# Kernel tuning notes

Measured on AMD Instinct MI355X. Metric: run time of the kernel, lower is better.

The kernel has to match this reference:

```python
import jax, jax.numpy as jnp
import numpy as np

N_ANCHORS = 25
N_CLASSES = 16
X_IMG = 296
Y_IMG = 296
OPLIST = ['conv','conv','MP','conv','conv','MP','conv','conv','conv','MP','conv','conv','conv','MP','conv','conv','conv']

def _size_list(s):
    out = [s]
    for op in OPLIST:
        out.append(out[-1] - 2 if op == 'conv' else out[-1] // 2)
    return out

XLIST = _size_list(X_IMG)  # ends at 7
YLIST = _size_list(Y_IMG)
FEAT = XLIST[-1]           # final feature-map size (7)
GRID = XLIST[-1] - 2       # anchor grid (5), source's xlist[-1]-2 convention
B, C = 2, 512


def setup_inputs() -> dict:
    key = jax.random.key(0)
    ks = jax.random.split(key, 12)
    D = C * 49
    return {
        'cfeats':   jax.random.normal(ks[0], (B, C, FEAT, FEAT), jnp.float32),
        'regcls':   jax.random.normal(ks[1], (B, 5, N_ANCHORS, GRID, GRID), jnp.float32) * 0.5,
        'wanchors': jax.random.uniform(ks[2], (N_ANCHORS, GRID, GRID), jnp.float32, 16.0, 128.0),
        'hanchors': jax.random.uniform(ks[3], (N_ANCHORS, GRID, GRID), jnp.float32, 16.0, 128.0),
        'xanchors': jax.random.uniform(ks[4], (N_ANCHORS, GRID, GRID), jnp.float32, 0.0, float(X_IMG)),
        'yanchors': jax.random.uniform(ks[5], (N_ANCHORS, GRID, GRID), jnp.float32, 0.0, float(Y_IMG)),
        'w1': jax.random.normal(ks[6], (200, D), jnp.float32) * 0.02,
        'b1': jnp.zeros((200,), jnp.float32),
        'w2': jax.random.normal(ks[7], (100, 200), jnp.float32) * 0.02,
        'b2': jnp.zeros((100,), jnp.float32),
        'w3': jax.random.normal(ks[8], (N_CLASSES + 1, 100), jnp.float32) * 0.02,
        'b3': jnp.zeros((N_CLASSES + 1,), jnp.float32),
        'w4': jax.random.normal(ks[9], (4 * (N_CLASSES + 1), 100), jnp.float32) * 0.02,
        'b4': jnp.zeros((4 * (N_CLASSES + 1),), jnp.float32),
    }


def _forward(cfeats, regcls, wanchors, hanchors, xanchors, yanchors,
             w1, b1, w2, b2, w3, b3, w4, b4):
    Bq, Cq, Fq, _ = cfeats.shape
    A, G = N_ANCHORS, GRID
    # ---- anchor-box decode ----
    wreg = jnp.exp(regcls[:, 2]) * wanchors
    hreg = jnp.exp(regcls[:, 3]) * hanchors
    xreg = regcls[:, 0] * wanchors + xanchors
    yreg = regcls[:, 1] * hanchors + yanchors
    xis = xreg - wreg / 2.0
    yis = yreg - hreg / 2.0
    xfs = xreg + wreg / 2.0
    yfs = yreg + hreg / 2.0
    c0 = jnp.floor(jax.nn.relu(xis))
    c1 = jnp.floor(jax.nn.relu(yis))
    c2 = jnp.minimum(jnp.ceil(xfs), float(X_IMG - 1))
    c3 = jnp.maximum(jnp.ceil(yfs), float(Y_IMG - 1))  # (sic) max, as in source
    valid = (xis < float(X_IMG)) & (yis < float(Y_IMG)) & (xfs >= 0.0) & (yfs >= 0.0)
    c4 = jnp.where(valid, jax.nn.sigmoid(regcls[:, 4]), 0.0)
    # ---- track coords through the conv/MP stack ----
    for i, op in enumerate(OPLIST):
        if op == 'conv':
            c0 = jax.nn.relu(c0 - 1.0)
            c1 = jax.nn.relu(c1 - 1.0)
            c2 = jnp.minimum(c2, float(XLIST[i + 1] - 1))
            c3 = jnp.minimum(c3, float(YLIST[i + 1] - 1))
        else:
            c0 = jnp.floor(c0 / 2.0); c1 = jnp.floor(c1 / 2.0)
            c2 = jnp.floor(c2 / 2.0); c3 = jnp.floor(c3 / 2.0)
    N = A * G * G  # flatten (anchor, x, y) -> roi index, same order as source
    xi = c0.reshape(Bq, N).astype(jnp.int32)
    yi = c1.reshape(Bq, N).astype(jnp.int32)
    xf = c2.reshape(Bq, N).astype(jnp.int32)
    yf = c3.reshape(Bq, N).astype(jnp.int32)
    roi_on = c4.reshape(Bq, N) > 0.0
    # ---- 7x7 RoIPool (vectorized; bins partition [xi, xf+1) via floor boundaries) ----
    ii = jnp.arange(8, dtype=jnp.int32)
    wx = xf + 1 - xi
    wy = yf + 1 - yi
    bx = xi[:, :, None] + (ii * wx[:, :, None]) // 7  # [B,N,8]
    by = yi[:, :, None] + (ii * wy[:, :, None]) // 7
    xs = jnp.arange(Fq, dtype=jnp.int32)
    maskx = (xs[None, None, None, :] >= bx[:, :, :7, None]) & (xs[None, None, None, :] < bx[:, :, 1:, None])  # [B,N,7,F]
    masky = (xs[None, None, None, :] >= by[:, :, :7, None]) & (xs[None, None, None, :] < by[:, :, 1:, None])
    NEG = jnp.float32(-1e30)
    feats_sg = jax.lax.stop_gradient(cfeats)
    # stage 1: max over x per bin i  -> val1/arg1: [B,N,7,C,F]
    val1 = jnp.full((Bq, N, 7, Cq, Fq), NEG, jnp.float32)
    arg1 = jnp.zeros((Bq, N, 7, Cq, Fq), jnp.int32)
    for x in range(Fq):
        cand = jnp.where(maskx[:, :, :, x][..., None, None], feats_sg[:, None, None, :, x, :], NEG)
        upd = cand > val1
        val1 = jnp.where(upd, cand, val1)
        arg1 = jnp.where(upd, x, arg1)
    # stage 2: max over y per bin j  -> val2/arg2: [B,N,7,7,C]
    val2 = jnp.full((Bq, N, 7, 7, Cq), NEG, jnp.float32)
    arg2 = jnp.zeros((Bq, N, 7, 7, Cq), jnp.int32)
    for y in range(Fq):
        cand = jnp.where(masky[:, :, None, :, y][..., None], val1[:, :, :, None, :, y], NEG)
        upd = cand > val2
        val2 = jnp.where(upd, cand, val2)
        arg2 = jnp.where(upd, y, arg2)
    # recover x index of the per-bin argmax, then one differentiable gather
    argx = jnp.take_along_axis(arg1[:, :, :, None, :, :], arg2[..., None], axis=-1)[..., 0]  # [B,N,7,7,C]
    cell = argx * Fq + arg2
    feats_flat = cfeats.reshape(Bq, Cq, Fq * Fq)
    pooled = jnp.take_along_axis(feats_flat[:, None, None, None, :, :], cell[..., None], axis=-1)[..., 0]
    keep = (val2 > NEG * 0.5) & roi_on[:, :, None, None, None]
    pooled = jnp.where(keep, pooled, 0.0)  # [B,N,7,7,C]
    # layout [..., C*49] with 49 = 7*i + j, matching source
    pooled = jnp.transpose(pooled, (0, 1, 4, 2, 3)).reshape(Bq, A, G, G, Cq * 49)
    # ---- MLP head ----
    z = jax.nn.relu(pooled @ w1.T + b1)
    z = jax.nn.relu(z @ w2.T + b2)
    z1 = z @ w3.T + b3
    z2 = z @ w4.T + b4
    K = N_CLASSES + 1
    z3 = jnp.stack([z2[..., 0:K], z2[..., K:2 * K], z2[..., 2 * K:3 * K], z2[..., 3 * K:4 * K]], axis=1)
    return z1, z3


def reference(cfeats, regcls, wanchors, hanchors, xanchors, yanchors,
              w1, b1, w2, b2, w3, b3, w4, b4):
    return _forward(cfeats, regcls, wanchors, hanchors, xanchors, yanchors,
                    w1, b1, w2, b2, w3, b3, w4, b4)
```

## Files before the change

kernel.cpp:

```cpp
#include <hip/hip_runtime.h>
#include <cstdint>

using short8 = __attribute__((ext_vector_type(8))) short;
using f32x4  = __attribute__((ext_vector_type(4))) float;

__device__ __forceinline__ uint16_t f2bf(float x) {
    uint32_t u = __float_as_uint(x);
    uint32_t r = (u + 0x7FFFu + ((u >> 16) & 1u)) >> 16;
    return (uint16_t)r;
}
__device__ __forceinline__ int fdiv7(int a) {
    int q = a / 7;
    if ((a % 7 != 0) && (a < 0)) q--;
    return q;
}

__global__ void __launch_bounds__(256) k_prep(const float* __restrict__ regcls,
                                              const float* __restrict__ wan,
                                              const float* __restrict__ han,
                                              const float* __restrict__ xan,
                                              const float* __restrict__ yan,
                                              const float* __restrict__ cf,
                                              const float* __restrict__ w1,
                                              const float* __restrict__ w2,
                                              const float* __restrict__ w3,
                                              const float* __restrict__ w4,
                                              int8_t* __restrict__ cells,
                                              uint16_t* __restrict__ cfb,
                                              uint16_t* __restrict__ w1f,
                                              float* __restrict__ w2t,
                                              float* __restrict__ w34t) {
    __shared__ float lds[16 * 804];
    int blk = blockIdx.x;
    int t = threadIdx.x;

    if (blk < 5) {
        int r = blk * 256 + t;
        if (r >= 1250) return;
        int b = r / 625, n = r - b * 625;
        const float* rc = regcls + b * 3125 + n;
        float t0 = rc[0], t1 = rc[625], t2 = rc[1250], t3 = rc[1875];
        float wa = wan[n], ha = han[n], xa = xan[n], ya = yan[n];
        float wr = expf(t2) * wa, hr = expf(t3) * ha;
        float xr = t0 * wa + xa, yr = t1 * ha + ya;
        float xis = xr - wr * 0.5f, yis = yr - hr * 0.5f;
        float xfs = xr + wr * 0.5f, yfs = yr + hr * 0.5f;
        bool valid = (xis < 296.f) && (yis < 296.f) && (xfs >= 0.f) && (yfs >= 0.f);
        int c0 = (int)floorf(fmaxf(xis, 0.f));
        int c1 = (int)floorf(fmaxf(yis, 0.f));
        int c2 = (int)fminf(ceilf(xfs), 295.f);
        int c3 = (int)fmaxf(ceilf(yfs), 295.f);
        const int  XL1[17]    = {294,292,146,144,142,71,69,67,65,32,30,28,26,13,11,9,7};
        const bool ISCONV[17] = {1,1,0,1,1,0,1,1,1,0,1,1,1,0,1,1,1};
        #pragma unroll
        for (int i = 0; i < 17; i++) {
            if (ISCONV[i]) {
                c0 = max(c0 - 1, 0); c1 = max(c1 - 1, 0);
                c2 = min(c2, XL1[i] - 1); c3 = min(c3, XL1[i] - 1);
            } else {
                c0 >>= 1; c1 >>= 1; c2 >>= 1; c3 >>= 1;
            }
        }
        int xi = c0, yi = c1, xf = c2, yf = c3;
        int wx = xf + 1 - xi, wy = yf + 1 - yi;
        int bx[8], by[8];
        #pragma unroll
        for (int i = 0; i < 8; i++) { bx[i] = xi + fdiv7(i * wx); by[i] = yi + fdiv7(i * wy); }
        int8_t* cr = cells + r * 64;
        #pragma unroll
        for (int i = 0; i < 7; i++)
            #pragma unroll
            for (int j = 0; j < 7; j++) {
                bool ne = valid && (bx[i + 1] > bx[i]) && (by[j + 1] > by[j]);
                cr[i * 7 + j] = ne ? (int8_t)(bx[i] * 7 + by[j]) : (int8_t)(-1);
            }
    } else if (blk < 37) {
        int g = (blk - 5) * 256 + t;
        int b = g >> 12;
        int xy = (g >> 6) & 63;
        int c0 = (g & 63) * 8;
        uint32_t pk[4];
        if (xy < 49) {
            #pragma unroll
            for (int h = 0; h < 4; h++) {
                uint16_t lo = f2bf(cf[(b * 512 + c0 + 2 * h) * 49 + xy]);
                uint16_t hi = f2bf(cf[(b * 512 + c0 + 2 * h + 1) * 49 + xy]);
                pk[h] = (uint32_t)lo | ((uint32_t)hi << 16);
            }
        } else {
            pk[0] = pk[1] = pk[2] = pk[3] = 0;
        }
        ((uint4*)cfb)[(b * 64 + xy) * 64 + (g & 63)] = make_uint4(pk[0], pk[1], pk[2], pk[3]);
    } else if (blk < 175) {
        int g = (blk - 37) * 256 + t;
        if (g < 200 * 128) {
            int k = g >> 7, o = g & 127;
            w2t[g] = (o < 100) ? w2[o * 200 + k] : 0.f;
        }
        int u = g - 200 * 128;
        if (u >= 0 && u < 100 * 96) {
            int k = u / 96, o = u - k * 96;
            float v = 0.f;
            if (o < 17) v = w3[o * 100 + k];
            else if (o < 85) v = w4[(o - 17) * 100 + k];
            w34t[u] = v;
        }
    } else {
        int idx = blk - 175;
        int nt = idx % 13, ct = idx / 13;
        int kbase = ct * 784;
        #pragma unroll 4
        for (int r = 0; r < 16; r++) {
            int o = nt * 16 + r;
            if (t < 196) {
                float4 v = make_float4(0.f, 0.f, 0.f, 0.f);
                if (o < 200) v = ((const float4*)(w1 + (size_t)o * 25088 + kbase))[t];
                *(float4*)&lds[r * 804 + 4 * t] = v;
            }
        }
        __syncthreads();
        int kc = ct >> 1;
        int q0 = (ct & 1) * 2;
        int lsub = t & 31;
        int l = q0 * 16 + lsub;
        int rrow = lsub & 15;
        int clbase = (lsub >> 4) * 8;
        for (int binb = 0; binb < 49; binb += 8) {
            int bin = binb + (t >> 5);
            if (bin < 49) {
                uint32_t pk[4];
                #pragma unroll
                for (int h = 0; h < 4; h++) {
                    uint16_t lo = f2bf(lds[rrow * 804 + (clbase + 2 * h) * 49 + bin]);
                    uint16_t hi = f2bf(lds[rrow * 804 + (clbase + 2 * h + 1) * 49 + bin]);
                    pk[h] = (uint32_t)lo | ((uint32_t)hi << 16);
                }
                ((uint4*)w1f)[((bin * 16 + kc) * 13 + nt) * 64 + l] =
                    make_uint4(pk[0], pk[1], pk[2], pk[3]);
            }
        }
    }
}

__global__ void __launch_bounds__(256) k_qgemm(const uint16_t* __restrict__ cfb,
                                               const uint16_t* __restrict__ w1f,
                                               float* __restrict__ Q) {
    __shared__ uint4 bs[16 * 64];
    int bin = blockIdx.x, nt = blockIdx.y;
    int t = threadIdx.x;
    const uint4* bw = (const uint4*)w1f + (bin * 208 + nt) * 64;
    for (int i = t; i < 16 * 64; i += 256) {
        int kc = i >> 6, l = i & 63;
        bs[i] = bw[kc * 832 + l];
    }
    __syncthreads();
    int w = t >> 6, l = t & 63;
    int r16 = l & 15, quad = l >> 4;
    int o = nt * 16 + r16;
    int xybase = w * 16 + quad * 4;
    #pragma unroll
    for (int b = 0; b < 2; b++) {
        const uint4* ap = (const uint4*)cfb + (b * 64 + w * 16 + r16) * 64 + quad;
        f32x4 acc = {0.f, 0.f, 0.f, 0.f};
        #pragma unroll
        for (int kc = 0; kc < 16; kc++) {
            uint4 av = ap[kc * 4];
            uint4 bv = bs[kc * 64 + l];
            short8 a8 = __builtin_bit_cast(short8, av);
            short8 b8 = __builtin_bit_cast(short8, bv);
            acc = __builtin_amdgcn_mfma_f32_16x16x32_bf16(a8, b8, acc, 0, 0, 0);
        }
        float* qb = Q + ((size_t)(b * 49 + bin) * 49) * 208 + o;
        #pragma unroll
        for (int reg = 0; reg < 4; reg++) {
            int xy = xybase + reg;
            if (xy < 49) qb[xy * 208] = acc[reg];
        }
    }
}

__global__ void __launch_bounds__(256) k_head(const int8_t* __restrict__ cells,
                                              const float* __restrict__ Q,
                                              const float* __restrict__ b1,
                                              const float* __restrict__ w2t,
                                              const float* __restrict__ b2,
                                              const float* __restrict__ w34t,
                                              const float* __restrict__ b3,
                                              const float* __restrict__ b4,
                                              float* __restrict__ out) {
    __shared__ float z1[200];
    __shared__ float z2[100];
    int r = blockIdx.x;
    int b = r / 625, n = r - b * 625;
    int t = threadIdx.x;
    const int8_t* cr = cells + r * 64;
    float s = 0.f;
    if (t < 208) {
        const float* qb = Q + (size_t)(b * 49) * 49 * 208 + t;
        #pragma unroll
        for (int bin = 0; bin < 49; bin++) {
            int cv = (int)cr[bin];
            int idx = max(cv, 0);
            float m = (cv >= 0) ? 1.f : 0.f;
            s += m * qb[(bin * 49 + idx) * 208];
        }
    }
    if (t < 200) z1[t] = fmaxf(s + b1[t], 0.f);
    __syncthreads();
    if (t < 100) {
        float a = b2[t];
        #pragma unroll 4
        for (int k = 0; k < 200; k++) a += z1[k] * w2t[k * 128 + t];
        z2[t] = fmaxf(a, 0.f);
    }
    __syncthreads();
    if (t < 85) {
        float a = (t < 17) ? b3[t] : b4[t - 17];
        #pragma unroll 4
        for (int k = 0; k < 100; k++) a += z2[k] * w34t[k * 96 + t];
        if (t < 17) {
            out[b * 10625 + n * 17 + t] = a;
        } else {
            int q = (t - 17) / 17, kk = (t - 17) - q * 17;
            out[21250 + b * 42500 + q * 10625 + n * 17 + kk] = a;
        }
    }
}

extern "C" void kernel_launch(void* const* d_in, const int* in_sizes, int n_in,
                              void* d_out, int out_size, void* d_ws, size_t ws_size,
                              hipStream_t stream) {
    const float* cfeats = (const float*)d_in[0];
    const float* regcls = (const float*)d_in[1];
    const float* wan    = (const float*)d_in[2];
    const float* han    = (const float*)d_in[3];
    const float* xan    = (const float*)d_in[4];
    const float* yan    = (const float*)d_in[5];
    const float* w1     = (const float*)d_in[6];
    const float* b1     = (const float*)d_in[7];
    const float* w2     = (const float*)d_in[8];
    const float* b2     = (const float*)d_in[9];
    const float* w3     = (const float*)d_in[10];
    const float* b3     = (const float*)d_in[11];
    const float* w4     = (const float*)d_in[12];
    const float* b4     = (const float*)d_in[13];

    char* ws = (char*)d_ws;
    int8_t*   cells = (int8_t*)ws;
    uint16_t* cfb   = (uint16_t*)(ws + 80000);
    uint16_t* w1f   = (uint16_t*)(ws + 211072);
    float*    Q     = (float*)(ws + 10647680);
    float*    w2t   = (float*)(ws + 14642944);
    float*    w34t  = (float*)(ws + 14745344);
    float*    out   = (float*)d_out;

    k_prep<<<dim3(591), dim3(256), 0, stream>>>(regcls, wan, han, xan, yan,
                                                cfeats, w1, w2, w3, w4,
                                                cells, cfb, w1f, w2t, w34t);
    k_qgemm<<<dim3(49, 13), dim3(256), 0, stream>>>(cfb, w1f, Q);
    k_head<<<dim3(1250), dim3(256), 0, stream>>>(cells, Q, b1, w2t, b2, w34t, b3, b4, out);
}
```

Measured before the change: 145.2 us.

## Fuse three kernels into one persistent kernel with grid-wide atomic barriers

```diff
diff --git a/kernel.cpp b/kernel.cpp
--- a/kernel.cpp
+++ b/kernel.cpp
@@ -15,214 +15,247 @@
     return q;
 }
 
-__global__ void __launch_bounds__(256) k_prep(const float* __restrict__ regcls,
-                                              const float* __restrict__ wan,
-                                              const float* __restrict__ han,
-                                              const float* __restrict__ xan,
-                                              const float* __restrict__ yan,
-                                              const float* __restrict__ cf,
-                                              const float* __restrict__ w1,
-                                              const float* __restrict__ w2,
-                                              const float* __restrict__ w3,
-                                              const float* __restrict__ w4,
-                                              int8_t* __restrict__ cells,
-                                              uint16_t* __restrict__ cfb,
-                                              uint16_t* __restrict__ w1f,
-                                              float* __restrict__ w2t,
-                                              float* __restrict__ w34t) {
-    __shared__ float lds[16 * 804];
-    int blk = blockIdx.x;
-    int t = threadIdx.x;
-
-    if (blk < 5) {
-        int r = blk * 256 + t;
-        if (r >= 1250) return;
-        int b = r / 625, n = r - b * 625;
-        const float* rc = regcls + b * 3125 + n;
-        float t0 = rc[0], t1 = rc[625], t2 = rc[1250], t3 = rc[1875];
-        float wa = wan[n], ha = han[n], xa = xan[n], ya = yan[n];
-        float wr = expf(t2) * wa, hr = expf(t3) * ha;
-        float xr = t0 * wa + xa, yr = t1 * ha + ya;
-        float xis = xr - wr * 0.5f, yis = yr - hr * 0.5f;
-        float xfs = xr + wr * 0.5f, yfs = yr + hr * 0.5f;
-        bool valid = (xis < 296.f) && (yis < 296.f) && (xfs >= 0.f) && (yfs >= 0.f);
-        int c0 = (int)floorf(fmaxf(xis, 0.f));
-        int c1 = (int)floorf(fmaxf(yis, 0.f));
-        int c2 = (int)fminf(ceilf(xfs), 295.f);
-        int c3 = (int)fmaxf(ceilf(yfs), 295.f);
-        const int  XL1[17]    = {294,292,146,144,142,71,69,67,65,32,30,28,26,13,11,9,7};
-        const bool ISCONV[17] = {1,1,0,1,1,0,1,1,1,0,1,1,1,0,1,1,1};
-        #pragma unroll
-        for (int i = 0; i < 17; i++) {
-            if (ISCONV[i]) {
-                c0 = max(c0 - 1, 0); c1 = max(c1 - 1, 0);
-                c2 = min(c2, XL1[i] - 1); c3 = min(c3, XL1[i] - 1);
+__device__ __forceinline__ void gbar(int* ctr, int target) {
+    __syncthreads();
+    if (threadIdx.x == 0) {
+        __threadfence_system();
+        __hip_atomic_fetch_add(ctr, 1, __ATOMIC_RELAXED, __HIP_MEMORY_SCOPE_SYSTEM);
+        int guard = 0;
+        while (__hip_atomic_load(ctr, __ATOMIC_RELAXED, __HIP_MEMORY_SCOPE_SYSTEM) < target) {
+            __builtin_amdgcn_s_sleep(1);
+            if (++guard > (1 << 27)) break;
+        }
+        __threadfence_system();
+    }
+    __syncthreads();
+}
+
+__global__ void __launch_bounds__(256, 2)
+k_fused(const float* __restrict__ regcls, const float* __restrict__ wan,
+        const float* __restrict__ han, const float* __restrict__ xan,
+        const float* __restrict__ yan, const float* __restrict__ cf,
+        const float* __restrict__ w1, const float* __restrict__ b1,
+        const float* __restrict__ w2, const float* __restrict__ b2,
+        const float* __restrict__ w3, const float* __restrict__ b3,
+        const float* __restrict__ w4, const float* __restrict__ b4,
+        int8_t* __restrict__ cells, uint16_t* __restrict__ cfb,
+        uint16_t* __restrict__ w1f, float* __restrict__ Q,
+        float* __restrict__ w2t, float* __restrict__ w34t,
+        int* __restrict__ bar, float* __restrict__ out)
+{
+    __shared__ __align__(16) char smem[16 * 788 * 2];
+    const int t = threadIdx.x;
+    const int nblk = gridDim.x;
+
+    for (int u = blockIdx.x; u < 591; u += nblk) {
+        if (u < 5) {
+            int r = u * 256 + t;
+            if (r < 1250) {
+                int b = r / 625, n = r - b * 625;
+                const float* rc = regcls + b * 3125 + n;
+                float t0 = rc[0], t1 = rc[625], t2 = rc[1250], t3 = rc[1875];
+                float wa = wan[n], ha = han[n], xa = xan[n], ya = yan[n];
+                float wr = expf(t2) * wa, hr = expf(t3) * ha;
+                float xr = t0 * wa + xa, yr = t1 * ha + ya;
+                float xis = xr - wr * 0.5f, yis = yr - hr * 0.5f;
+                float xfs = xr + wr * 0.5f, yfs = yr + hr * 0.5f;
+                bool valid = (xis < 296.f) && (yis < 296.f) && (xfs >= 0.f) && (yfs >= 0.f);
+                int c0 = (int)floorf(fmaxf(xis, 0.f));
+                int c1 = (int)floorf(fmaxf(yis, 0.f));
+                int c2 = (int)fminf(ceilf(xfs), 295.f);
+                int c3 = (int)fmaxf(ceilf(yfs), 295.f);
+                const int  XL1[17]    = {294,292,146,144,142,71,69,67,65,32,30,28,26,13,11,9,7};
+                const bool ISCONV[17] = {1,1,0,1,1,0,1,1,1,0,1,1,1,0,1,1,1};
+                #pragma unroll
+                for (int i = 0; i < 17; i++) {
+                    if (ISCONV[i]) {
+                        c0 = max(c0 - 1, 0); c1 = max(c1 - 1, 0);
+                        c2 = min(c2, XL1[i] - 1); c3 = min(c3, XL1[i] - 1);
+                    } else {
+                        c0 >>= 1; c1 >>= 1; c2 >>= 1; c3 >>= 1;
+                    }
+                }
+                int xi = c0, yi = c1, xf = c2, yf = c3;
+                int wx = xf + 1 - xi, wy = yf + 1 - yi;
+                int bx[8], by[8];
+                #pragma unroll
+                for (int i = 0; i < 8; i++) { bx[i] = xi + fdiv7(i * wx); by[i] = yi + fdiv7(i * wy); }
+                int8_t* crw = cells + r * 64;
+                #pragma unroll
+                for (int i = 0; i < 7; i++)
+                    #pragma unroll
+                    for (int j = 0; j < 7; j++) {
+                        bool ne = valid && (bx[i + 1] > bx[i]) && (by[j + 1] > by[j]);
+                        crw[i * 7 + j] = ne ? (int8_t)(bx[i] * 7 + by[j]) : (int8_t)(-1);
+                    }
+            }
+        } else if (u < 37) {
+            int g = (u - 5) * 256 + t;
+            int b = g >> 12;
+            int xy = (g >> 6) & 63;
+            int c0 = (g & 63) * 8;
+            uint32_t pk[4];
+            if (xy < 49) {
+                #pragma unroll
+                for (int h = 0; h < 4; h++) {
+                    uint16_t lo = f2bf(cf[(b * 512 + c0 + 2 * h) * 49 + xy]);
+                    uint16_t hi = f2bf(cf[(b * 512 + c0 + 2 * h + 1) * 49 + xy]);
+                    pk[h] = (uint32_t)lo | ((uint32_t)hi << 16);
+                }
             } else {
-                c0 >>= 1; c1 >>= 1; c2 >>= 1; c3 >>= 1;
-            }
-        }
-        int xi = c0, yi = c1, xf = c2, yf = c3;
-        int wx = xf + 1 - xi, wy = yf + 1 - yi;
-        int bx[8], by[8];
-        #pragma unroll
-        for (int i = 0; i < 8; i++) { bx[i] = xi + fdiv7(i * wx); by[i] = yi + fdiv7(i * wy); }
-        int8_t* cr = cells + r * 64;
-        #pragma unroll
-        for (int i = 0; i < 7; i++)
+                pk[0] = pk[1] = pk[2] = pk[3] = 0;
+            }
+            ((uint4*)cfb)[(b * 64 + xy) * 64 + (g & 63)] = make_uint4(pk[0], pk[1], pk[2], pk[3]);
+        } else if (u < 175) {
+            int g = (u - 37) * 256 + t;
+            if (g < 200 * 128) {
+                int k = g >> 7, o = g & 127;
+                w2t[g] = (o < 100) ? w2[o * 200 + k] : 0.f;
+            }
+            int uu = g - 200 * 128;
+            if (uu >= 0 && uu < 100 * 96) {
+                int k = uu / 96, o = uu - k * 96;
+                float v = 0.f;
+                if (o < 17) v = w3[o * 100 + k];
+                else if (o < 85) v = w4[(o - 17) * 100 + k];
+                w34t[uu] = v;
+            }
+        } else {
+            uint16_t* lh = (uint16_t*)smem;
+            __syncthreads();
+            int idx = u - 175;
+            int nt = idx % 13, ct = idx / 13;
+            int kbase = ct * 784;
+            #pragma unroll 4
+            for (int rr = 0; rr < 16; rr++) {
+                int o = nt * 16 + rr;
+                if (t < 196) {
+                    float4 v = make_float4(0.f, 0.f, 0.f, 0.f);
+                    if (o < 200) v = ((const float4*)(w1 + (size_t)o * 25088 + kbase))[t];
+                    ushort4 hv;
+                    hv.x = f2bf(v.x); hv.y = f2bf(v.y); hv.z = f2bf(v.z); hv.w = f2bf(v.w);
+                    *(ushort4*)&lh[rr * 788 + 4 * t] = hv;
+                }
+            }
+            __syncthreads();
+            int kc = ct >> 1;
+            int q0 = (ct & 1) * 2;
+            int lsub = t & 31;
+            int l = q0 * 16 + lsub;
+            int rrow = lsub & 15;
+            int clbase = (lsub >> 4) * 8;
+            for (int binb = 0; binb < 49; binb += 8) {
+                int bin = binb + (t >> 5);
+                if (bin < 49) {
+                    uint32_t pk[4];
+                    #pragma unroll
+                    for (int h = 0; h < 4; h++) {
+                        uint32_t lo = lh[rrow * 788 + (clbase + 2 * h) * 49 + bin];
+                        uint32_t hi = lh[rrow * 788 + (clbase + 2 * h + 1) * 49 + bin];
+                        pk[h] = lo | (hi << 16);
+                    }
+                    ((uint4*)w1f)[((bin * 16 + kc) * 13 + nt) * 64 + l] =
+                        make_uint4(pk[0], pk[1], pk[2], pk[3]);
+                }
+            }
+        }
+    }
+    gbar(bar, nblk);
+
+    {
+        uint4* bs = (uint4*)smem;
+        for (int u = blockIdx.x; u < 637; u += nblk) {
+            int bin = u % 49, nt = u / 49;
+            __syncthreads();
+            const uint4* bw = (const uint4*)w1f + (bin * 208 + nt) * 64;
+            for (int i = t; i < 16 * 64; i += 256) {
+                int kc = i >> 6, l = i & 63;
+                bs[i] = bw[kc * 832 + l];
+            }
+            __syncthreads();
+            int w = t >> 6, l = t & 63;
+            int r16 = l & 15, quad = l >> 4;
+            int o = nt * 16 + r16;
+            int xybase = w * 16 + quad * 4;
             #pragma unroll
-            for (int j = 0; j < 7; j++) {
-                bool ne = valid && (bx[i + 1] > bx[i]) && (by[j + 1] > by[j]);
-                cr[i * 7 + j] = ne ? (int8_t)(bx[i] * 7 + by[j]) : (int8_t)(-1);
-            }
-    } else if (blk < 37) {
-        int g = (blk - 5) * 256 + t;
-        int b = g >> 12;
-        int xy = (g >> 6) & 63;
-        int c0 = (g & 63) * 8;
-        uint32_t pk[4];
-        if (xy < 49) {
-            #pragma unroll
-            for (int h = 0; h < 4; h++) {
-                uint16_t lo = f2bf(cf[(b * 512 + c0 + 2 * h) * 49 + xy]);
-                uint16_t hi = f2bf(cf[(b * 512 + c0 + 2 * h + 1) * 49 + xy]);
-                pk[h] = (uint32_t)lo | ((uint32_t)hi << 16);
-            }
-        } else {
-            pk[0] = pk[1] = pk[2] = pk[3] = 0;
-        }
-        ((uint4*)cfb)[(b * 64 + xy) * 64 + (g & 63)] = make_uint4(pk[0], pk[1], pk[2], pk[3]);
-    } else if (blk < 175) {
-        int g = (blk - 37) * 256 + t;
-        if (g < 200 * 128) {
-            int k = g >> 7, o = g & 127;
-            w2t[g] = (o < 100) ? w2[o * 200 + k] : 0.f;
-        }
-        int u = g - 200 * 128;
-        if (u >= 0 && u < 100 * 96) {
-            int k = u / 96, o = u - k * 96;
-            float v = 0.f;
-            if (o < 17) v = w3[o * 100 + k];
-            else if (o < 85) v = w4[(o - 17) * 100 + k];
-            w34t[u] = v;
-        }
-    } else {
-        int idx = blk - 175;
-        int nt = idx % 13, ct = idx / 13;
-        int kbase = ct * 784;
-        #pragma unroll 4
-        for (int r = 0; r < 16; r++) {
-            int o = nt * 16 + r;
-            if (t < 196) {
-                float4 v = make_float4(0.f, 0.f, 0.f, 0.f);
-                if (o < 200) v = ((const float4*)(w1 + (size_t)o * 25088 + kbase))[t];
-                *(float4*)&lds[r * 804 + 4 * t] = v;
-            }
-        }
-        __syncthreads();
-        int kc = ct >> 1;
-        int q0 = (ct & 1) * 2;
-        int lsub = t & 31;
-        int l = q0 * 16 + lsub;
-        int rrow = lsub & 15;
-        int clbase = (lsub >> 4) * 8;
-        for (int binb = 0; binb < 49; binb += 8) {
-            int bin = binb + (t >> 5);
-            if (bin < 49) {
-                uint32_t pk[4];
-                #pragma unroll
-                for (int h = 0; h < 4; h++) {
-                    uint16_t lo = f2bf(lds[rrow * 804 + (clbase + 2 * h) * 49 + bin]);
-                    uint16_t hi = f2bf(lds[rrow * 804 + (clbase + 2 * h + 1) * 49 + bin]);
-                    pk[h] = (uint32_t)lo | ((uint32_t)hi << 16);
-                }
-                ((uint4*)w1f)[((bin * 16 + kc) * 13 + nt) * 64 + l] =
-                    make_uint4(pk[0], pk[1], pk[2], pk[3]);
-            }
-        }
-    }
-}
-
-__global__ void __launch_bounds__(256) k_qgemm(const uint16_t* __restrict__ cfb,
-                                               const uint16_t* __restrict__ w1f,
-                                               float* __restrict__ Q) {
-    __shared__ uint4 bs[16 * 64];
-    int bin = blockIdx.x, nt = blockIdx.y;
-    int t = threadIdx.x;
-    const uint4* bw = (const uint4*)w1f + (bin * 208 + nt) * 64;
-    for (int i = t; i < 16 * 64; i += 256) {
-        int kc = i >> 6, l = i & 63;
-        bs[i] = bw[kc * 832 + l];
-    }
-    __syncthreads();
-    int w = t >> 6, l = t & 63;
-    int r16 = l & 15, quad = l >> 4;
-    int o = nt * 16 + r16;
-    int xybase = w * 16 + quad * 4;
-    #pragma unroll
-    for (int b = 0; b < 2; b++) {
-        const uint4* ap = (const uint4*)cfb + (b * 64 + w * 16 + r16) * 64 + quad;
-        f32x4 acc = {0.f, 0.f, 0.f, 0.f};
-        #pragma unroll
-        for (int kc = 0; kc < 16; kc++) {
-            uint4 av = ap[kc * 4];
-            uint4 bv = bs[kc * 64 + l];
-            short8 a8 = __builtin_bit_cast(short8, av);
-            short8 b8 = __builtin_bit_cast(short8, bv);
-            acc = __builtin_amdgcn_mfma_f32_16x16x32_bf16(a8, b8, acc, 0, 0, 0);
-        }
-        float* qb = Q + ((size_t)(b * 49 + bin) * 49) * 208 + o;
-        #pragma unroll
-        for (int reg = 0; reg < 4; reg++) {
-            int xy = xybase + reg;
-            if (xy < 49) qb[xy * 208] = acc[reg];
-        }
-    }
-}
-
-__global__ void __launch_bounds__(256) k_head(const int8_t* __restrict__ cells,
-                                              const float* __restrict__ Q,
-                                              const float* __restrict__ b1,
-                                              const float* __restrict__ w2t,
-                                              const float* __restrict__ b2,
-                                              const float* __restrict__ w34t,
-                                              const float* __restrict__ b3,
-                                              const float* __restrict__ b4,
-                                              float* __restrict__ out) {
-    __shared__ float z1[200];
-    __shared__ float z2[100];
-    int r = blockIdx.x;
-    int b = r / 625, n = r - b * 625;
-    int t = threadIdx.x;
-    const int8_t* cr = cells + r * 64;
-    float s = 0.f;
-    if (t < 208) {
-        const float* qb = Q + (size_t)(b * 49) * 49 * 208 + t;
-        #pragma unroll
-        for (int bin = 0; bin < 49; bin++) {
-            int cv = (int)cr[bin];
-            int idx = max(cv, 0);
-            float m = (cv >= 0) ? 1.f : 0.f;
-            s += m * qb[(bin * 49 + idx) * 208];
-        }
-    }
-    if (t < 200) z1[t] = fmaxf(s + b1[t], 0.f);
-    __syncthreads();
-    if (t < 100) {
-        float a = b2[t];
-        #pragma unroll 4
-        for (int k = 0; k < 200; k++) a += z1[k] * w2t[k * 128 + t];
-        z2[t] = fmaxf(a, 0.f);
-    }
-    __syncthreads();
-    if (t < 85) {
-        float a = (t < 17) ? b3[t] : b4[t - 17];
-        #pragma unroll 4
-        for (int k = 0; k < 100; k++) a += z2[k] * w34t[k * 96 + t];
-        if (t < 17) {
-            out[b * 10625 + n * 17 + t] = a;
-        } else {
-            int q = (t - 17) / 17, kk = (t - 17) - q * 17;
-            out[21250 + b * 42500 + q * 10625 + n * 17 + kk] = a;
+            for (int b = 0; b < 2; b++) {
+                const uint4* ap = (const uint4*)cfb + (b * 64 + w * 16 + r16) * 64 + quad;
+                f32x4 acc = {0.f, 0.f, 0.f, 0.f};
+                #pragma unroll
+                for (int kc = 0; kc < 16; kc++) {
+                    uint4 av = ap[kc * 4];
+                    uint4 bv = bs[kc * 64 + l];
+                    short8 a8 = __builtin_bit_cast(short8, av);
+                    short8 b8 = __builtin_bit_cast(short8, bv);
+                    acc = __builtin_amdgcn_mfma_f32_16x16x32_bf16(a8, b8, acc, 0, 0, 0);
+                }
+                float* qb = Q + ((size_t)(b * 49 + bin) * 49) * 208 + o;
+                #pragma unroll
+                for (int reg = 0; reg < 4; reg++) {
+                    int xy = xybase + reg;
+                    if (xy < 49) qb[xy * 208] = acc[reg];
+                }
+            }
+        }
+    }
+    gbar(bar, 2 * nblk);
+
+    {
+        float* z1 = (float*)smem;
+        float* z2 = (float*)smem + 256;
+        float* zp = (float*)smem + 384;
+        int o2 = t & 127, kq = t >> 7;
+        for (int u = blockIdx.x; u < 1250; u += nblk) {
+            int b = u / 625, n = u - b * 625;
+            const int8_t* cr = cells + u * 64;
+            float s0 = 0.f, s1 = 0.f;
+            if (t < 208) {
+                const float* qb = Q + (size_t)(b * 49) * 49 * 208 + t;
+                #pragma unroll
+                for (int bin = 0; bin < 49; bin++) {
+                    int cv = (int)cr[bin];
+                    int iidx = max(cv, 0);
+                    float m = (cv >= 0) ? 1.f : 0.f;
+                    float v = m * qb[(bin * 49 + iidx) * 208];
+                    if (bin & 1) s1 += v; else s0 += v;
+                }
+            }
+            __syncthreads();
+            if (t < 200) z1[t] = fmaxf(s0 + s1 + b1[t], 0.f);
+            __syncthreads();
+            float a0 = 0.f, a1 = 0.f;
+            if (o2 < 100) {
+                const float* wp = w2t + (kq * 100) * 128 + o2;
+                const float* zz = z1 + kq * 100;
+                #pragma unroll 10
+                for (int k = 0; k < 100; k += 2) {
+                    a0 += zz[k]     * wp[k * 128];
+                    a1 += zz[k + 1] * wp[(k + 1) * 128];
+                }
+            }
+            zp[t] = a0 + a1;
+            __syncthreads();
+            if (t < 100) z2[t] = fmaxf(b2[t] + zp[t] + zp[t + 128], 0.f);
+            __syncthreads();
+            float c0 = 0.f;
+            if (o2 < 85) {
+                const float* wp = w34t + (kq * 50) * 96 + o2;
+                const float* zz = z2 + kq * 50;
+                #pragma unroll 10
+                for (int k = 0; k < 50; k++) c0 += zz[k] * wp[k * 96];
+            }
+            zp[t] = c0;
+            __syncthreads();
+            if (t < 85) {
+                float v = ((t < 17) ? b3[t] : b4[t - 17]) + zp[t] + zp[t + 128];
+                if (t < 17) {
+                    out[b * 10625 + n * 17 + t] = v;
+                } else {
+                    int q = (t - 17) / 17, kk = (t - 17) - q * 17;
+                    out[21250 + b * 42500 + q * 10625 + n * 17 + kk] = v;
+                }
+            }
+            __syncthreads();
         }
     }
 }
@@ -252,11 +285,11 @@
     float*    Q     = (float*)(ws + 10647680);
     float*    w2t   = (float*)(ws + 14642944);
     float*    w34t  = (float*)(ws + 14745344);
-    float*    out   = (float*)d_out;
-
-    k_prep<<<dim3(591), dim3(256), 0, stream>>>(regcls, wan, han, xan, yan,
-                                                cfeats, w1, w2, w3, w4,
-                                                cells, cfb, w1f, w2t, w34t);
-    k_qgemm<<<dim3(49, 13), dim3(256), 0, stream>>>(cfb, w1f, Q);
-    k_head<<<dim3(1250), dim3(256), 0, stream>>>(cells, Q, b1, w2t, b2, w34t, b3, b4, out);
-}
+    int*      bar   = (int*)(ws + 14783744);
+    float*    outp  = (float*)d_out;
+
+    (void)hipMemsetAsync(bar, 0, 16, stream);
+    k_fused<<<dim3(512), dim3(256), 0, stream>>>(
+        regcls, wan, han, xan, yan, cfeats, w1, b1, w2, b2, w3, b3, w4, b4,
+        cells, cfb, w1f, Q, w2t, w34t, bar, outp);
+}
```

New measurement: 265.5 us. +82.9%, slower.
